# Performance work log

Measured on AMD Instinct MI355X. Metric: run time of the kernel, lower is better.

## Reference

```python
import jax, jax.numpy as jnp
import numpy as np

N_NODES = 100000
DIM_IN = 128
N_PAIRS = 500000
D2 = 2 * DIM_IN  # concat dim = 256


def setup_inputs() -> dict:
    key = jax.random.key(0)
    k_x, k_idx, k_w1, k_b1, k_w2, k_b2 = jax.random.split(key, 6)
    x = jax.random.normal(k_x, (N_NODES, DIM_IN), dtype=jnp.float32)
    junc_index_pair = jax.random.randint(k_idx, (N_PAIRS, 2), 0, N_NODES, dtype=jnp.int64)
    # MLP: Linear(2d -> 2d) + ReLU, then Linear(2d -> 1), both with bias
    s1 = 1.0 / np.sqrt(D2)
    W1 = jax.random.uniform(k_w1, (D2, D2), minval=-s1, maxval=s1, dtype=jnp.float32)
    b1 = jax.random.uniform(k_b1, (D2,), minval=-s1, maxval=s1, dtype=jnp.float32)
    W2 = jax.random.uniform(k_w2, (D2, 1), minval=-s1, maxval=s1, dtype=jnp.float32)
    b2 = jax.random.uniform(k_b2, (1,), minval=-s1, maxval=s1, dtype=jnp.float32)
    return {"x": x, "junc_index_pair": junc_index_pair,
            "W1": W1, "b1": b1, "W2": W2, "b2": b2}


def reference(x, junc_index_pair, W1, b1, W2, b2):
    # gather both endpoints: [n_pairs, dim_in] each
    node_start = x[junc_index_pair[:, 0]]
    node_end = x[junc_index_pair[:, 1]]
    h = jnp.concatenate((node_start, node_end), axis=1)  # [n_pairs, 2*dim_in]
    h = jax.nn.relu(h @ W1 + b1)                          # [n_pairs, 2*dim_in]
    pred = h @ W2 + b2                                    # [n_pairs, 1]
    return pred.squeeze()                                 # [n_pairs]
```

## Files before the change

### kernel.cpp

```cpp
#include <hip/hip_runtime.h>
#include <hip/hip_bf16.h>
#include <stdint.h>

#define NPAIRS 500000
#define NNODES 100000
#define DIM    128
#define D2     256

typedef __bf16 bf16;
typedef __bf16 bf16x8 __attribute__((ext_vector_type(8)));
typedef float  f32x4  __attribute__((ext_vector_type(4)));

__global__ void pack_w1p(const float* __restrict__ W1, bf16* __restrict__ w1p) {
    int t = blockIdx.x * 256 + threadIdx.x;
    int lane = t & 63;
    int kks = (t >> 6) & 3;
    int cg  = t >> 8;
    int l15 = lane & 15, lg = lane >> 4;
    int np = cg * 16 + l15;
    int k0 = kks * 32 + lg * 8;
    const float* src = (np < D2) ? (W1 + (long)k0 * D2 + np)
                                 : (W1 + (long)(k0 + 128) * D2 + (np - D2));
    bf16x8 v;
#pragma unroll
    for (int j = 0; j < 8; ++j) v[j] = (bf16)src[(long)j * D2];
    *(bf16x8*)((char*)w1p + ((long)t << 4)) = v;
}

__launch_bounds__(512, 8)
__global__ void gemm_uvq(const float* __restrict__ x,
                         const bf16*  __restrict__ w1p,
                         int8_t*      __restrict__ UV8,
                         float*       __restrict__ Sq) {
    __shared__ char xt[64 * 256];
    __shared__ char hs8[64 * 128];
    __shared__ int  smx[64];
    int tid  = threadIdx.x;
    int wave = tid >> 6, lane = tid & 63;
    int l15 = lane & 15, lg = lane >> 4;
    long nb = (long)blockIdx.x * 64;

#pragma unroll
    for (int it = 0; it < 2; ++it) {
        int task = it * 512 + tid;
        int r = task >> 4, c = task & 15;
        long node = nb + r;
        const float* src = x + (node < NNODES ? node : 0) * DIM + c * 8;
        float4 a = ((const float4*)src)[0];
        float4 b = ((const float4*)src)[1];
        bf16x8 v;
        v[0]=(bf16)a.x; v[1]=(bf16)a.y; v[2]=(bf16)a.z; v[3]=(bf16)a.w;
        v[4]=(bf16)b.x; v[5]=(bf16)b.y; v[6]=(bf16)b.z; v[7]=(bf16)b.w;
        *(bf16x8*)(xt + r * 256 + ((c * 16) ^ ((r & 15) << 4))) = v;
    }
    __syncthreads();

#pragma unroll 1
    for (int p = 0; p < 4; ++p) {
        if (tid < 64) smx[tid] = 0;

        f32x4 acc[4];
#pragma unroll
        for (int nf = 0; nf < 4; ++nf) acc[nf] = (f32x4){0.f, 0.f, 0.f, 0.f};

        int cg = p * 8 + wave;
#pragma unroll
        for (int kks = 0; kks < 4; ++kks) {
            bf16x8 wf = *(const bf16x8*)((const char*)w1p +
                            (((cg * 4 + kks) * 64 + lane) << 4));
            int kbyte = kks * 64 + lg * 16;
#pragma unroll
            for (int nf = 0; nf < 4; ++nf) {
                int r = nf * 16 + l15;
                bf16x8 xf = *(const bf16x8*)(xt + r * 256 + (kbyte ^ ((r & 15) << 4)));
                acc[nf] = __builtin_amdgcn_mfma_f32_16x16x32_bf16(wf, xf, acc[nf], 0, 0, 0);
            }
        }
        __syncthreads();

#pragma unroll
        for (int nf = 0; nf < 4; ++nf) {
            float m = fmaxf(fmaxf(fabsf(acc[nf][0]), fabsf(acc[nf][1])),
                            fmaxf(fabsf(acc[nf][2]), fabsf(acc[nf][3])));
            m = fmaxf(m, __shfl_xor(m, 16));
            m = fmaxf(m, __shfl_xor(m, 32));
            if (lg == 0) atomicMax(&smx[nf * 16 + l15], __float_as_int(m));
        }
        __syncthreads();

#pragma unroll
        for (int nf = 0; nf < 4; ++nf) {
            int row = nf * 16 + l15;
            float m2 = __int_as_float(smx[row]);
            float rs = (m2 > 1e-20f) ? 127.0f * __builtin_amdgcn_rcpf(m2) : 0.f;
            uint32_t packed = 0;
#pragma unroll
            for (int r = 0; r < 4; ++r) {
                int q = (int)__builtin_rintf(acc[nf][r] * rs);
                q = q > 127 ? 127 : (q < -127 ? -127 : q);
                packed |= ((uint32_t)(q & 255)) << (8 * r);
            }
            int col = (wave * 16 + lg * 4) ^ ((row & 7) << 4);
            *(uint32_t*)(hs8 + row * 128 + col) = packed;
        }
        __syncthreads();

        {
            int row = tid >> 3, c16 = (tid & 7) << 4;
            uint4 v = *(const uint4*)(hs8 + row * 128 + (c16 ^ ((row & 7) << 4)));
            long node = nb + row;
            if (node < NNODES)
                *(uint4*)((char*)UV8 + node * 512 + p * 128 + c16) = v;
        }
        if (tid < 64) {
            long node = nb + tid;
            if (node < NNODES)
                Sq[node * 4 + p] = __int_as_float(smx[tid]) * (1.0f / 127.0f);
        }
    }
}

__launch_bounds__(512)
__global__ void pair_pred8(const int8_t* __restrict__ UV8,
                           const float* __restrict__ Sq,
                           const int* __restrict__ junc,
                           const float* __restrict__ b1, const float* __restrict__ w2,
                           const float* __restrict__ b2, float* __restrict__ out) {
    int tid = threadIdx.x;
    int l15 = tid & 15;
    long qid = (((long)blockIdx.x * 512 + tid) >> 4);
    int st = l15 >> 3;
    float b1c[16], w2c[16];
#pragma unroll
    for (int e = 0; e < 16; ++e) {
        int col = l15 * 16 + e;
        b1c[e] = b1[col];
        w2c[e] = w2[col];
    }
    float b2v = b2[0];
    for (long p = qid; p < NPAIRS; p += 32768) {
        int2 ij = ((const int2*)junc)[p];
        uint4 u4 = *(const uint4*)(UV8 + (long)ij.x * 512 + l15 * 16);
        uint4 v4 = *(const uint4*)(UV8 + (long)ij.y * 512 + 256 + l15 * 16);
        float su = Sq[ij.x * 4 + st];
        float sv = Sq[ij.y * 4 + 2 + st];
        float s = 0.f;
#define DEC(ud, vd, eb)                                                        \
        {                                                                      \
            _Pragma("unroll")                                                  \
            for (int b = 0; b < 4; ++b) {                                      \
                int ub = (int)((ud) << (24 - 8 * b)) >> 24;                    \
                int vb = (int)((vd) << (24 - 8 * b)) >> 24;                    \
                float h = fmaf(su, (float)ub, fmaf(sv, (float)vb, b1c[(eb) + b])); \
                s = fmaf(fmaxf(h, 0.f), w2c[(eb) + b], s);                     \
            }                                                                  \
        }
        DEC(u4.x, v4.x, 0)
        DEC(u4.y, v4.y, 4)
        DEC(u4.z, v4.z, 8)
        DEC(u4.w, v4.w, 12)
#undef DEC
        s += __shfl_xor(s, 1);
        s += __shfl_xor(s, 2);
        s += __shfl_xor(s, 4);
        s += __shfl_xor(s, 8);
        if (l15 == 0) out[p] = s + b2v;
    }
}

__global__ void pack_w1(const float* __restrict__ W1, bf16* __restrict__ w1f) {
    int t = blockIdx.x * 256 + threadIdx.x;
    int lane = t & 63;
    int kk = (t >> 6) & 7;
    int cg = t >> 9;
    int l15 = lane & 15, lg = lane >> 4;
    bf16x8 v;
#pragma unroll
    for (int j = 0; j < 8; ++j)
        v[j] = (bf16)W1[(long)(kk * 32 + lg * 8 + j) * D2 + cg * 16 + l15];
    *(bf16x8*)((char*)w1f + ((long)t << 4)) = v;
}

__launch_bounds__(512, 2)
__global__ void fused_fb(const float* __restrict__ x, const int* __restrict__ junc,
                         const bf16* __restrict__ w1f, const float* __restrict__ b1,
                         const float* __restrict__ w2p, const float* __restrict__ b2,
                         float* __restrict__ out) {
    __shared__ char  atile[128 * 512];
    __shared__ float outp[4][128];
    int tid  = threadIdx.x;
    int wave = tid >> 6, lane = tid & 63;
    int l15 = lane & 15, lg = lane >> 4;
    int wr = wave >> 2, wc = wave & 3;
    long base_p = (long)blockIdx.x * 128;

    float bb[4][4], ww[4][4];
#pragma unroll
    for (int m = 0; m < 4; ++m)
#pragma unroll
        for (int r = 0; r < 4; ++r) {
            int hc = wc * 64 + m * 16 + lg * 4 + r;
            bb[m][r] = b1[hc];
            ww[m][r] = w2p[hc];
        }
#pragma unroll
    for (int it = 0; it < 8; ++it) {
        int task  = it * 512 + tid;
        int nr = task >> 4, chunk = task & 15;
        int r = nr >> 1, side = nr & 1;
        long p = base_p + r;
        int idx = (p < NPAIRS) ? junc[p * 2 + side] : 0;
        const float4* src = (const float4*)(x + (long)idx * DIM + chunk * 8);
        float4 a = src[0], b = src[1];
        bf16x8 v;
        v[0]=(bf16)a.x; v[1]=(bf16)a.y; v[2]=(bf16)a.z; v[3]=(bf16)a.w;
        v[4]=(bf16)b.x; v[5]=(bf16)b.y; v[6]=(bf16)b.z; v[7]=(bf16)b.w;
        int bir = side * 256 + chunk * 16;
        *(bf16x8*)(atile + r * 512 + (bir ^ ((r & 31) << 4))) = v;
    }
    __syncthreads();

    f32x4 acc[4][4];
#pragma unroll
    for (int m = 0; m < 4; ++m)
#pragma unroll
        for (int n = 0; n < 4; ++n)
            acc[m][n] = (f32x4){0.f, 0.f, 0.f, 0.f};
#pragma unroll
    for (int kk = 0; kk < 8; ++kk) {
        bf16x8 xf[4];
        int kbyte = kk * 64 + lg * 16;
#pragma unroll
        for (int n = 0; n < 4; ++n) {
            int r = wr * 64 + n * 16 + l15;
            xf[n] = *(const bf16x8*)(atile + r * 512 + (kbyte ^ ((r & 31) << 4)));
        }
#pragma unroll
        for (int m = 0; m < 4; ++m) {
            bf16x8 wf = *(const bf16x8*)((const char*)w1f +
                            ((((wc * 4 + m) * 8 + kk) * 64 + lane) << 4));
#pragma unroll
            for (int n = 0; n < 4; ++n)
                acc[m][n] = __builtin_amdgcn_mfma_f32_16x16x32_bf16(wf, xf[n], acc[m][n], 0, 0, 0);
        }
    }
#pragma unroll
    for (int n = 0; n < 4; ++n) {
        float s = 0.f;
#pragma unroll
        for (int m = 0; m < 4; ++m)
#pragma unroll
            for (int r = 0; r < 4; ++r)
                s = fmaf(fmaxf(acc[m][n][r] + bb[m][r], 0.f), ww[m][r], s);
        s += __shfl_xor(s, 16);
        s += __shfl_xor(s, 32);
        if (lg == 0) outp[wc][wr * 64 + n * 16 + l15] = s;
    }
    __syncthreads();
    if (tid < 128) {
        long p = base_p + tid;
        if (p < NPAIRS)
            out[p] = b2[0] + outp[0][tid] + outp[1][tid] + outp[2][tid] + outp[3][tid];
    }
}

extern "C" void kernel_launch(void* const* d_in, const int* in_sizes, int n_in,
                              void* d_out, int out_size, void* d_ws, size_t ws_size,
                              hipStream_t stream) {
    const float* x    = (const float*)d_in[0];
    const int*   junc = (const int*)  d_in[1];
    const float* W1   = (const float*)d_in[2];
    const float* b1   = (const float*)d_in[3];
    const float* W2   = (const float*)d_in[4];
    const float* b2   = (const float*)d_in[5];
    float* out = (float*)d_out;

    const size_t UV8_B = (size_t)NNODES * 512;
    const size_t SQ_B  = (size_t)NNODES * 16;
    const size_t NEED  = UV8_B + SQ_B + 131072;

    if (ws_size >= NEED) {
        char* base = (char*)d_ws;
        int8_t* UV8 = (int8_t*)base;
        float*  Sq  = (float*)(base + UV8_B);
        bf16*   w1p = (bf16*) (base + UV8_B + SQ_B);
        hipLaunchKernelGGL(pack_w1p, dim3(32), dim3(256), 0, stream, W1, w1p);
        hipLaunchKernelGGL(gemm_uvq, dim3((NNODES + 63) / 64), dim3(512), 0, stream,
                           x, w1p, UV8, Sq);
        hipLaunchKernelGGL(pair_pred8, dim3(1024), dim3(512), 0, stream,
                           UV8, Sq, junc, b1, W2, b2, out);
    } else {
        bf16* w1f = (bf16*)d_ws;
        hipLaunchKernelGGL(pack_w1, dim3(32), dim3(256), 0, stream, W1, w1f);
        hipLaunchKernelGGL(fused_fb, dim3((NPAIRS + 127) / 128), dim3(512), 0, stream,
                           x, junc, w1f, b1, W2, b2, out);
    }
}
```

Before: 93.58 us.

## Quantize per 256-column half instead of 128-column quarters in node GEMM

The node GEMM now processes two halves of 256 output columns, each wave computing two column groups per pass, instead of four passes of 128 columns. This halves the number of barrier and reduce/quantize phases and reuses each LDS x fragment for two MFMAs. The int8 scale is now per node per half, so the pair kernel loads one scale per endpoint and the scale buffer shrinks. Coarser scale groups may reduce quantization accuracy, and the extra accumulators raise register pressure.

After: 107.5 us. +14.8%, slower.

```diff
diff --git a/kernel.cpp b/kernel.cpp
--- a/kernel.cpp
+++ b/kernel.cpp
@@ -31,14 +31,16 @@
 __global__ void gemm_uvq(const float* __restrict__ x,
                          const bf16*  __restrict__ w1p,
                          int8_t*      __restrict__ UV8,
-                         float*       __restrict__ Sq) {
+                         float*       __restrict__ Sq2) {
     __shared__ char xt[64 * 256];
-    __shared__ char hs8[64 * 128];
+    __shared__ char hs16[64 * 256];
     __shared__ int  smx[64];
     int tid  = threadIdx.x;
     int wave = tid >> 6, lane = tid & 63;
     int l15 = lane & 15, lg = lane >> 4;
     long nb = (long)blockIdx.x * 64;
+
+    if (tid < 64) smx[tid] = 0;
 
 #pragma unroll
     for (int it = 0; it < 2; ++it) {
@@ -56,32 +58,39 @@
     __syncthreads();
 
 #pragma unroll 1
-    for (int p = 0; p < 4; ++p) {
-        if (tid < 64) smx[tid] = 0;
-
-        f32x4 acc[4];
-#pragma unroll
-        for (int nf = 0; nf < 4; ++nf) acc[nf] = (f32x4){0.f, 0.f, 0.f, 0.f};
-
-        int cg = p * 8 + wave;
+    for (int h = 0; h < 2; ++h) {
+        f32x4 acc[2][4];
+#pragma unroll
+        for (int m = 0; m < 2; ++m)
+#pragma unroll
+            for (int nf = 0; nf < 4; ++nf)
+                acc[m][nf] = (f32x4){0.f, 0.f, 0.f, 0.f};
+
+        int cg0 = h * 16 + wave * 2;
 #pragma unroll
         for (int kks = 0; kks < 4; ++kks) {
-            bf16x8 wf = *(const bf16x8*)((const char*)w1p +
-                            (((cg * 4 + kks) * 64 + lane) << 4));
+            bf16x8 wf0 = *(const bf16x8*)((const char*)w1p +
+                             ((((cg0    ) * 4 + kks) * 64 + lane) << 4));
+            bf16x8 wf1 = *(const bf16x8*)((const char*)w1p +
+                             ((((cg0 + 1) * 4 + kks) * 64 + lane) << 4));
             int kbyte = kks * 64 + lg * 16;
 #pragma unroll
             for (int nf = 0; nf < 4; ++nf) {
                 int r = nf * 16 + l15;
                 bf16x8 xf = *(const bf16x8*)(xt + r * 256 + (kbyte ^ ((r & 15) << 4)));
-                acc[nf] = __builtin_amdgcn_mfma_f32_16x16x32_bf16(wf, xf, acc[nf], 0, 0, 0);
+                acc[0][nf] = __builtin_amdgcn_mfma_f32_16x16x32_bf16(wf0, xf, acc[0][nf], 0, 0, 0);
+                acc[1][nf] = __builtin_amdgcn_mfma_f32_16x16x32_bf16(wf1, xf, acc[1][nf], 0, 0, 0);
             }
         }
         __syncthreads();
 
 #pragma unroll
         for (int nf = 0; nf < 4; ++nf) {
-            float m = fmaxf(fmaxf(fabsf(acc[nf][0]), fabsf(acc[nf][1])),
-                            fmaxf(fabsf(acc[nf][2]), fabsf(acc[nf][3])));
+            float m = fmaxf(
+                fmaxf(fmaxf(fabsf(acc[0][nf][0]), fabsf(acc[0][nf][1])),
+                      fmaxf(fabsf(acc[0][nf][2]), fabsf(acc[0][nf][3]))),
+                fmaxf(fmaxf(fabsf(acc[1][nf][0]), fabsf(acc[1][nf][1])),
+                      fmaxf(fabsf(acc[1][nf][2]), fabsf(acc[1][nf][3]))));
             m = fmaxf(m, __shfl_xor(m, 16));
             m = fmaxf(m, __shfl_xor(m, 32));
             if (lg == 0) atomicMax(&smx[nf * 16 + l15], __float_as_int(m));
@@ -93,43 +102,48 @@
             int row = nf * 16 + l15;
             float m2 = __int_as_float(smx[row]);
             float rs = (m2 > 1e-20f) ? 127.0f * __builtin_amdgcn_rcpf(m2) : 0.f;
-            uint32_t packed = 0;
-#pragma unroll
-            for (int r = 0; r < 4; ++r) {
-                int q = (int)__builtin_rintf(acc[nf][r] * rs);
-                q = q > 127 ? 127 : (q < -127 ? -127 : q);
-                packed |= ((uint32_t)(q & 255)) << (8 * r);
+#pragma unroll
+            for (int m = 0; m < 2; ++m) {
+                uint32_t packed = 0;
+#pragma unroll
+                for (int r = 0; r < 4; ++r) {
+                    int q = (int)__builtin_rintf(acc[m][nf][r] * rs);
+                    q = q > 127 ? 127 : (q < -127 ? -127 : q);
+                    packed |= ((uint32_t)(q & 255)) << (8 * r);
+                }
+                int col = (wave * 32 + m * 16 + lg * 4) ^ ((row & 15) << 4);
+                *(uint32_t*)(hs16 + row * 256 + col) = packed;
             }
-            int col = (wave * 16 + lg * 4) ^ ((row & 7) << 4);
-            *(uint32_t*)(hs8 + row * 128 + col) = packed;
         }
         __syncthreads();
 
-        {
-            int row = tid >> 3, c16 = (tid & 7) << 4;
-            uint4 v = *(const uint4*)(hs8 + row * 128 + (c16 ^ ((row & 7) << 4)));
+#pragma unroll
+        for (int it = 0; it < 2; ++it) {
+            int ci = it * 512 + tid;
+            int row = ci >> 4, c16 = (ci & 15) << 4;
+            uint4 v = *(const uint4*)(hs16 + row * 256 + (c16 ^ ((row & 15) << 4)));
             long node = nb + row;
             if (node < NNODES)
-                *(uint4*)((char*)UV8 + node * 512 + p * 128 + c16) = v;
+                *(uint4*)((char*)UV8 + node * 512 + h * 256 + c16) = v;
         }
         if (tid < 64) {
             long node = nb + tid;
             if (node < NNODES)
-                Sq[node * 4 + p] = __int_as_float(smx[tid]) * (1.0f / 127.0f);
+                Sq2[node * 2 + h] = __int_as_float(smx[tid]) * (1.0f / 127.0f);
+            smx[tid] = 0;
         }
     }
 }
 
 __launch_bounds__(512)
 __global__ void pair_pred8(const int8_t* __restrict__ UV8,
-                           const float* __restrict__ Sq,
+                           const float* __restrict__ Sq2,
                            const int* __restrict__ junc,
                            const float* __restrict__ b1, const float* __restrict__ w2,
                            const float* __restrict__ b2, float* __restrict__ out) {
     int tid = threadIdx.x;
     int l15 = tid & 15;
     long qid = (((long)blockIdx.x * 512 + tid) >> 4);
-    int st = l15 >> 3;
     float b1c[16], w2c[16];
 #pragma unroll
     for (int e = 0; e < 16; ++e) {
@@ -142,8 +156,8 @@
         int2 ij = ((const int2*)junc)[p];
         uint4 u4 = *(const uint4*)(UV8 + (long)ij.x * 512 + l15 * 16);
         uint4 v4 = *(const uint4*)(UV8 + (long)ij.y * 512 + 256 + l15 * 16);
-        float su = Sq[ij.x * 4 + st];
-        float sv = Sq[ij.y * 4 + 2 + st];
+        float su = Sq2[ij.x * 2];
+        float sv = Sq2[ij.y * 2 + 1];
         float s = 0.f;
 #define DEC(ud, vd, eb)                                                        \
         {                                                                      \
@@ -276,19 +290,19 @@
     float* out = (float*)d_out;
 
     const size_t UV8_B = (size_t)NNODES * 512;
-    const size_t SQ_B  = (size_t)NNODES * 16;
+    const size_t SQ_B  = (size_t)NNODES * 8;
     const size_t NEED  = UV8_B + SQ_B + 131072;
 
     if (ws_size >= NEED) {
         char* base = (char*)d_ws;
         int8_t* UV8 = (int8_t*)base;
-        float*  Sq  = (float*)(base + UV8_B);
+        float*  Sq2 = (float*)(base + UV8_B);
         bf16*   w1p = (bf16*) (base + UV8_B + SQ_B);
         hipLaunchKernelGGL(pack_w1p, dim3(32), dim3(256), 0, stream, W1, w1p);
         hipLaunchKernelGGL(gemm_uvq, dim3((NNODES + 63) / 64), dim3(512), 0, stream,
-                           x, w1p, UV8, Sq);
+                           x, w1p, UV8, Sq2);
         hipLaunchKernelGGL(pair_pred8, dim3(1024), dim3(512), 0, stream,
-                           UV8, Sq, junc, b1, W2, b2, out);
+                           UV8, Sq2, junc, b1, W2, b2, out);
     } else {
         bf16* w1f = (bf16*)d_ws;
         hipLaunchKernelGGL(pack_w1, dim3(32), dim3(256), 0, stream, W1, w1f);
```
